# Performance work log

Hardware: AMD Instinct MI355X
Metric: run time of the kernel (lower is better)

Reference implementation:

```python
import jax, jax.numpy as jnp
import numpy as np

EPS = 1e-06


def setup_inputs() -> dict:
    key = jax.random.key(0)
    ks = jax.random.split(key, 6)
    B, H, S, W = 1, 12, 768, 32
    attn_logits = jax.random.normal(ks[0], (B, H, S, S), dtype=jnp.float32)
    # shared first linear: Linear(1, mlp_width) -> weight [W,1], bias [W]
    W_in = jax.random.normal(ks[1], (W, 1), dtype=jnp.float32) * (1.0)
    b_in = jax.random.normal(ks[2], (W,), dtype=jnp.float32) * 0.1
    # per-head output linear: Linear(mlp_width, 1) -> weight [H, W], bias [H]
    W_out = jax.random.normal(ks[3], (H, W), dtype=jnp.float32) / np.sqrt(W)
    b_out = jax.random.normal(ks[4], (H,), dtype=jnp.float32) * 0.1
    c = jnp.asarray(0.1, dtype=jnp.float32)
    L_multiplier = jnp.asarray(1.0, dtype=jnp.float32)
    init_L = jnp.asarray(512.0, dtype=jnp.float32)  # requires_grad=False in torch
    return {"attn_logits": attn_logits, "W_in": W_in, "b_in": b_in,
            "W_out": W_out, "b_out": b_out, "c": c,
            "L_multiplier": L_multiplier, "init_L": init_L}


def reference(attn_logits, W_in, b_in, W_out, b_out, c, L_multiplier, init_L):
    # gates and reverse cumulative sum along the key axis
    gates = jax.nn.sigmoid(attn_logits)                      # [B,H,S,S]
    pos = jax.lax.cumsum(gates, axis=3, reverse=True)        # flip-cumsum-flip
    numerator = jnp.log(jnp.abs(c * pos) + 1.0)
    max_pos = pos[..., 0:1]                                  # [B,H,S,1]
    threshold = jnp.abs(L_multiplier * init_L)
    denominator = jnp.log(jnp.abs(c * jnp.minimum(max_pos, threshold)) + 1.0) + EPS
    dist = numerator / denominator                           # [B,H,S,S]
    # shared Linear(1,W) + ReLU, then per-head Linear(W,1)
    w1 = W_in[:, 0]                                          # [W]
    hidden = jax.nn.relu(dist[..., None] * w1 + b_in)        # [B,H,S,S,W]
    fire_bias = jnp.einsum('bhijw,hw->bhij', hidden, W_out) + b_out[None, :, None, None]
    return fire_bias
```

## Files before the change

kernel.cpp:

```cpp
#include <hip/hip_runtime.h>
#include <math.h>

#define EPS_F 1e-6f
#define S_DIM 768
#define W_DIM 32
#define H_DIM 12
#define NK 33


__global__ __launch_bounds__(512) void cope_setup_kernel(
    const float* __restrict__ W_in, const float* __restrict__ b_in,
    const float* __restrict__ W_out, const float* __restrict__ b_out,
    float* __restrict__ ws)
{
    __shared__ float th[W_DIM];
    __shared__ int   rk[W_DIM];
    const int t = threadIdx.x;

    if (t < W_DIM) {
        float w1 = W_in[t], b = b_in[t];
        th[t] = (w1 != 0.0f) ? (-b / w1) : __builtin_inff();
    }
    __syncthreads();

    if (t < W_DIM) {
        float mine = th[t];
        int r = 0;
        for (int v = 0; v < W_DIM; v++) {
            float o = th[v];
            if (o < mine || (o == mine && v < t)) r++;
        }
        rk[t] = r;
        ws[r] = mine;
    }
    __syncthreads();

    if (t < H_DIM * NK) {
        int h = t / NK, k = t % NK;
        float A = 0.0f, B = b_out[h];
        for (int w = 0; w < W_DIM; w++) {
            float w1 = W_in[w], bv = b_in[w], ov = W_out[h * W_DIM + w];
            bool active = (w1 > 0.0f) ? (k > rk[w])
                        : (w1 < 0.0f) ? (k <= rk[w])
                        : (bv > 0.0f);
            if (active) { A += w1 * ov; B += bv * ov; }
        }
        ws[W_DIM + h * 2 * NK + 2 * k]     = A;
        ws[W_DIM + h * 2 * NK + 2 * k + 1] = B;
    }
}

__global__ __launch_bounds__(256) void cope_fire_kernel(
    const float* __restrict__ attn,
    const float* __restrict__ c_p,
    const float* __restrict__ Lm_p,
    const float* __restrict__ iL_p,
    const float* __restrict__ ws,
    float* __restrict__ out)
{
    const int t    = threadIdx.x;
    const int lane = t & 63;
    const int wave = t >> 6;
    const int row  = blockIdx.x * 4 + wave;
    const int h    = blockIdx.x / (S_DIM / 4);

    __shared__ float  sh[1 + W_DIM];
    __shared__ float2 sAB[NK];

    if (t == 0)     sh[0] = -__builtin_inff();
    if (t < W_DIM)  sh[1 + t] = ws[t];
    if (t < NK) {
        const float* p = ws + W_DIM + h * 2 * NK + 2 * t;
        sAB[t] = make_float2(p[0], p[1]);
    }

    const float u16 = ws[15];
    const float u8a = ws[7],  u8b = ws[23];
    const float u4a = ws[3],  u4b = ws[11], u4c = ws[19], u4d = ws[27];
    const float c   = c_p[0];
    const float thr = fabsf(Lm_p[0] * iL_p[0]);

    const float* rowp = attn + (size_t)row * S_DIM + lane * 12;
    float4 v0 = *(const float4*)(rowp);
    float4 v1 = *(const float4*)(rowp + 4);
    float4 v2 = *(const float4*)(rowp + 8);
    float g[12] = { v0.x, v0.y, v0.z, v0.w, v1.x, v1.y, v1.z, v1.w,
                    v2.x, v2.y, v2.z, v2.w };
#pragma unroll
    for (int i = 0; i < 12; i++)
        g[i] = __builtin_amdgcn_rcpf(1.0f + __expf(-g[i]));

    float T0 = 0.0f;
#pragma unroll
    for (int i = 0; i < 12; i++) T0 += g[i];
    float P = T0;
#pragma unroll
    for (int d = 1; d < 64; d <<= 1) {
        float y = __shfl_up(P, d, 64);
        if (lane >= d) P += y;
    }
    const float total = __shfl(P, 63, 64);
    const float base  = total - P + T0;

    const float den     = __logf(fabsf(c * fminf(total, thr)) + 1.0f) + EPS_F;
    const float inv_den = __builtin_amdgcn_rcpf(den);

    float e = 0.0f;
#pragma unroll
    for (int i = 0; i < 12; i++) {
        float pos = base - e;
        e += g[i];
        g[i] = __logf(fabsf(c * pos) + 1.0f) * inv_den;
    }

    __syncthreads();

    float d0 = g[0];
    int k = 0;
    if (u16 < d0) k = 16;
    float l2 = (k != 0) ? u8b : u8a;
    if (l2 < d0) k += 8;
    float l3ab = (k & 8) ? u4b : u4a;
    float l3cd = (k & 8) ? u4d : u4c;
    float l3   = (k & 16) ? l3cd : l3ab;
    if (l3 < d0) k += 4;
    if (sh[k + 2] < d0) k += 2;
    if (sh[k + 1] < d0) k += 1;
    if (sh[k + 1] < d0) k += 1;

    float o[12];
    {
        float2 ab = sAB[k];
        o[0] = fmaf(d0, ab.x, ab.y);
    }
#pragma unroll
    for (int i = 1; i < 12; i++) {
        float d = g[i];
        if (sh[k] >= d) k--;
        while (sh[k] >= d) k--;
        float2 ab = sAB[k];
        o[i] = fmaf(d, ab.x, ab.y);
    }

    float* op = out + (size_t)row * S_DIM + lane * 12;
    *(float4*)(op)     = make_float4(o[0], o[1], o[2],  o[3]);
    *(float4*)(op + 4) = make_float4(o[4], o[5], o[6],  o[7]);
    *(float4*)(op + 8) = make_float4(o[8], o[9], o[10], o[11]);
}

extern "C" void kernel_launch(void* const* d_in, const int* in_sizes, int n_in,
                              void* d_out, int out_size, void* d_ws, size_t ws_size,
                              hipStream_t stream) {
    const float* attn  = (const float*)d_in[0];
    const float* W_in  = (const float*)d_in[1];
    const float* b_in  = (const float*)d_in[2];
    const float* W_out = (const float*)d_in[3];
    const float* b_out = (const float*)d_in[4];
    const float* c_p   = (const float*)d_in[5];
    const float* Lm_p  = (const float*)d_in[6];
    const float* iL_p  = (const float*)d_in[7];
    float* out = (float*)d_out;
    float* ws  = (float*)d_ws;

    cope_setup_kernel<<<1, 512, 0, stream>>>(W_in, b_in, W_out, b_out, ws);

    const int rows = H_DIM * S_DIM;
    cope_fire_kernel<<<rows / 4, 256, 0, stream>>>(
        attn, c_p, Lm_p, iL_p, ws, out);
}
```

Baseline: 105.0 us.

## Fuse piecewise-linear table setup into fire kernel and use per-element binary search

Removes the separate single-block setup kernel: each block now computes the sorted ReLU breakpoints and its head's per-segment slope/intercept table in shared memory, overlapping this with the global row load. This drops a kernel launch and the dependency between the two kernels. The sequential downward walk from the first element's segment is replaced by an independent branchless binary search for every element, which removes data-dependent while loops at the cost of extra shared-memory lookups. Every block redundantly runs the 32x32 rank sort and the 33x32 table build.

```diff
diff --git a/kernel.cpp b/kernel.cpp
--- a/kernel.cpp
+++ b/kernel.cpp
@@ -8,54 +8,15 @@
 #define NK 33
 
 
-__global__ __launch_bounds__(512) void cope_setup_kernel(
-    const float* __restrict__ W_in, const float* __restrict__ b_in,
-    const float* __restrict__ W_out, const float* __restrict__ b_out,
-    float* __restrict__ ws)
-{
-    __shared__ float th[W_DIM];
-    __shared__ int   rk[W_DIM];
-    const int t = threadIdx.x;
-
-    if (t < W_DIM) {
-        float w1 = W_in[t], b = b_in[t];
-        th[t] = (w1 != 0.0f) ? (-b / w1) : __builtin_inff();
-    }
-    __syncthreads();
-
-    if (t < W_DIM) {
-        float mine = th[t];
-        int r = 0;
-        for (int v = 0; v < W_DIM; v++) {
-            float o = th[v];
-            if (o < mine || (o == mine && v < t)) r++;
-        }
-        rk[t] = r;
-        ws[r] = mine;
-    }
-    __syncthreads();
-
-    if (t < H_DIM * NK) {
-        int h = t / NK, k = t % NK;
-        float A = 0.0f, B = b_out[h];
-        for (int w = 0; w < W_DIM; w++) {
-            float w1 = W_in[w], bv = b_in[w], ov = W_out[h * W_DIM + w];
-            bool active = (w1 > 0.0f) ? (k > rk[w])
-                        : (w1 < 0.0f) ? (k <= rk[w])
-                        : (bv > 0.0f);
-            if (active) { A += w1 * ov; B += bv * ov; }
-        }
-        ws[W_DIM + h * 2 * NK + 2 * k]     = A;
-        ws[W_DIM + h * 2 * NK + 2 * k + 1] = B;
-    }
-}
-
 __global__ __launch_bounds__(256) void cope_fire_kernel(
     const float* __restrict__ attn,
+    const float* __restrict__ W_in,
+    const float* __restrict__ b_in,
+    const float* __restrict__ W_out,
+    const float* __restrict__ b_out,
     const float* __restrict__ c_p,
     const float* __restrict__ Lm_p,
     const float* __restrict__ iL_p,
-    const float* __restrict__ ws,
     float* __restrict__ out)
 {
     const int t    = threadIdx.x;
@@ -64,26 +25,57 @@
     const int row  = blockIdx.x * 4 + wave;
     const int h    = blockIdx.x / (S_DIM / 4);
 
+    __shared__ float  s_w1[W_DIM], s_bin[W_DIM], s_wout[W_DIM];
+    __shared__ float  s_th[W_DIM];
+    __shared__ int    s_rk[W_DIM];
     __shared__ float  sh[1 + W_DIM];
     __shared__ float2 sAB[NK];
-
-    if (t == 0)     sh[0] = -__builtin_inff();
-    if (t < W_DIM)  sh[1 + t] = ws[t];
-    if (t < NK) {
-        const float* p = ws + W_DIM + h * 2 * NK + 2 * t;
-        sAB[t] = make_float2(p[0], p[1]);
-    }
-
-    const float u16 = ws[15];
-    const float u8a = ws[7],  u8b = ws[23];
-    const float u4a = ws[3],  u4b = ws[11], u4c = ws[19], u4d = ws[27];
-    const float c   = c_p[0];
-    const float thr = fabsf(Lm_p[0] * iL_p[0]);
 
     const float* rowp = attn + (size_t)row * S_DIM + lane * 12;
     float4 v0 = *(const float4*)(rowp);
     float4 v1 = *(const float4*)(rowp + 4);
     float4 v2 = *(const float4*)(rowp + 8);
+
+    const float c   = c_p[0];
+    const float thr = fabsf(Lm_p[0] * iL_p[0]);
+    const float bo  = b_out[h];
+
+    if (t < W_DIM) {
+        float w1 = W_in[t];
+        float bv = b_in[t];
+        s_w1[t]   = w1;
+        s_bin[t]  = bv;
+        s_wout[t] = W_out[h * W_DIM + t];
+        s_th[t]   = (w1 != 0.0f) ? (-bv / w1) : __builtin_inff();
+    }
+    if (t == 64) sh[0] = -__builtin_inff();
+    __syncthreads();
+
+    if (t < W_DIM) {
+        float mine = s_th[t];
+        int r = 0;
+        for (int v = 0; v < W_DIM; v++) {
+            float o = s_th[v];
+            if (o < mine || (o == mine && v < t)) r++;
+        }
+        s_rk[t] = r;
+        sh[1 + r] = mine;
+    }
+    __syncthreads();
+
+    if (t < NK) {
+        float A = 0.0f, B = bo;
+        for (int w = 0; w < W_DIM; w++) {
+            float w1 = s_w1[w], bv = s_bin[w], ov = s_wout[w];
+            int   r  = s_rk[w];
+            bool active = (w1 > 0.0f) ? (t > r)
+                        : (w1 < 0.0f) ? (t <= r)
+                        : (bv > 0.0f);
+            if (active) { A = fmaf(w1, ov, A); B = fmaf(bv, ov, B); }
+        }
+        sAB[t] = make_float2(A, B);
+    }
+
     float g[12] = { v0.x, v0.y, v0.z, v0.w, v1.x, v1.y, v1.z, v1.w,
                     v2.x, v2.y, v2.z, v2.w };
 #pragma unroll
@@ -115,29 +107,25 @@
 
     __syncthreads();
 
-    float d0 = g[0];
-    int k = 0;
-    if (u16 < d0) k = 16;
-    float l2 = (k != 0) ? u8b : u8a;
-    if (l2 < d0) k += 8;
-    float l3ab = (k & 8) ? u4b : u4a;
-    float l3cd = (k & 8) ? u4d : u4c;
-    float l3   = (k & 16) ? l3cd : l3ab;
-    if (l3 < d0) k += 4;
-    if (sh[k + 2] < d0) k += 2;
-    if (sh[k + 1] < d0) k += 1;
-    if (sh[k + 1] < d0) k += 1;
+    const float u16 = sh[16];
+    const float u8a = sh[8],  u8b = sh[24];
+    const float u4a = sh[4],  u4b = sh[12], u4c = sh[20], u4d = sh[28];
 
     float o[12];
-    {
-        float2 ab = sAB[k];
-        o[0] = fmaf(d0, ab.x, ab.y);
-    }
 #pragma unroll
-    for (int i = 1; i < 12; i++) {
+    for (int i = 0; i < 12; i++) {
         float d = g[i];
-        if (sh[k] >= d) k--;
-        while (sh[k] >= d) k--;
+        int k = 0;
+        if (u16 < d) k = 16;
+        float l2 = (k != 0) ? u8b : u8a;
+        if (l2 < d) k += 8;
+        float l3ab = (k & 8) ? u4b : u4a;
+        float l3cd = (k & 8) ? u4d : u4c;
+        float l3   = (k & 16) ? l3cd : l3ab;
+        if (l3 < d) k += 4;
+        if (sh[k + 2] < d) k += 2;
+        if (sh[k + 1] < d) k += 1;
+        if (sh[k + 1] < d) k += 1;
         float2 ab = sAB[k];
         o[i] = fmaf(d, ab.x, ab.y);
     }
@@ -160,11 +148,8 @@
     const float* Lm_p  = (const float*)d_in[6];
     const float* iL_p  = (const float*)d_in[7];
     float* out = (float*)d_out;
-    float* ws  = (float*)d_ws;
-
-    cope_setup_kernel<<<1, 512, 0, stream>>>(W_in, b_in, W_out, b_out, ws);
 
     const int rows = H_DIM * S_DIM;
     cope_fire_kernel<<<rows / 4, 256, 0, stream>>>(
-        attn, c_p, Lm_p, iL_p, ws, out);
+        attn, W_in, b_in, W_out, b_out, c_p, Lm_p, iL_p, out);
 }
```

After: 112.3 us. 1.07x slower.
